# Optimization experiments

Hardware: AMD Instinct MI355X
Metric: run time of the kernel (lower is better)

Reference implementation:

```python
import jax, jax.numpy as jnp
import numpy as np

DIM = 1024
HEADS = 16
DIM_HEAD = 64
INNER = HEADS * DIM_HEAD  # 1024
MAX_LEN = 4096
BASE = 10000.0
EPS = 1.1920928955078125e-07  # torch.finfo(float32).eps (RMSNorm eps=None default)


def _rope_tables():
    t = np.arange(MAX_LEN, dtype=np.float32)
    inv_freq = 1.0 / (BASE ** (np.arange(0, DIM_HEAD, 2, dtype=np.float32) / DIM_HEAD))
    freqs = np.einsum('i,j->ij', t, inv_freq)          # [max_len, d/2]
    emb = np.concatenate([freqs, freqs], axis=-1)       # [max_len, d]
    return jnp.asarray(np.sin(emb)), jnp.asarray(np.cos(emb))


def setup_inputs() -> dict:
    key = jax.random.key(0)
    ks = jax.random.split(key, 5)
    x = jax.random.normal(ks[0], (2, 2048, DIM), dtype=jnp.float32)
    norm_w = jnp.ones((DIM,), dtype=jnp.float32)
    # store projection weights as [in, out] (transposed torch Linear weight)
    w_qkv = jax.random.normal(ks[1], (DIM, 3 * INNER), dtype=jnp.float32) * (DIM ** -0.5)
    w_o = jax.random.normal(ks[2], (INNER, DIM), dtype=jnp.float32) * (INNER ** -0.5)
    b_o = jax.random.normal(ks[3], (DIM,), dtype=jnp.float32) * 0.01
    sin, cos = _rope_tables()
    return {"x": x, "norm_w": norm_w, "w_qkv": w_qkv, "w_o": w_o, "b_o": b_o,
            "sin": sin, "cos": cos}


def _rotate_half(t):
    t1, t2 = jnp.split(t, 2, axis=-1)
    return jnp.concatenate([-t2, t1], axis=-1)


def _apply_rope(t, sin, cos):
    # t: [b, h, n, d]; sin/cos: [n, d]
    return t * cos + _rotate_half(t) * sin


def reference(x, norm_w, w_qkv, w_o, b_o, sin, cos):
    b, n, _ = x.shape
    # RMSNorm
    xn = x * jax.lax.rsqrt(jnp.mean(x * x, axis=-1, keepdims=True) + EPS) * norm_w
    # QKV projection
    qkv = xn @ w_qkv                                   # [b, n, 3*inner]
    q, k, v = jnp.split(qkv, 3, axis=-1)
    def to_heads(t):
        return t.reshape(b, n, HEADS, DIM_HEAD).transpose(0, 2, 1, 3)  # [b,h,n,d]
    q, k, v = to_heads(q), to_heads(k), to_heads(v)
    s, c = sin[:n], cos[:n]
    q = _apply_rope(q, s, c)
    k = _apply_rope(k, s, c)
    # causal SDPA
    scale = DIM_HEAD ** -0.5
    scores = jnp.einsum('bhqd,bhkd->bhqk', q, k) * scale
    causal = jnp.tril(jnp.ones((n, n), dtype=bool))
    scores = jnp.where(causal, scores, jnp.finfo(scores.dtype).min)
    attn = jax.nn.softmax(scores, axis=-1)
    out = jnp.einsum('bhqk,bhkd->bhqd', attn, v)
    out = out.transpose(0, 2, 1, 3).reshape(b, n, INNER)
    return out @ w_o + b_o
```

## Files before the change

### kernel.cpp

```cpp
#include <hip/hip_runtime.h>
#include <hip/hip_bf16.h>
#include <stdint.h>
#include <stddef.h>

#define NTOK   2048
#define NHEAD  16
#define DHEAD  64
#define DMODEL 1024
#define NROWS  4096
#define NQKV   3072
#define RMS_EPS 1.1920928955078125e-07f
#define QSCALE 0.1803368801111204f

typedef short bf16x8 __attribute__((ext_vector_type(8)));
typedef float f32x4  __attribute__((ext_vector_type(4)));
typedef unsigned short u16x4 __attribute__((ext_vector_type(4)));
typedef unsigned short u16x8 __attribute__((ext_vector_type(8)));

__device__ __forceinline__ unsigned short f2b(float f) {
  unsigned u = __builtin_bit_cast(unsigned, f);
  return (unsigned short)((u + 0x7fffu + ((u >> 16) & 1u)) >> 16);
}

__device__ __forceinline__ unsigned pk2bf(float a, float b) {
  __hip_bfloat162 h = __float22bfloat162_rn(make_float2(a, b));
  unsigned u;
  __builtin_memcpy(&u, &h, 4);
  return u;
}

__device__ __forceinline__ void gl16(const void* g, void* l) {
  __builtin_amdgcn_global_load_lds((__attribute__((address_space(1))) void*)g,
                                   (__attribute__((address_space(3))) void*)l,
                                   16, 0, 0);
}

__global__ __launch_bounds__(256) void k_rmsnorm(const float* __restrict__ x,
                                                 const float* __restrict__ w,
                                                 unsigned short* __restrict__ xn) {
  int row = blockIdx.x;
  int t = threadIdx.x;
  float4 v = ((const float4*)(x + (size_t)row * DMODEL))[t];
  float ss = v.x * v.x + v.y * v.y + v.z * v.z + v.w * v.w;
#pragma unroll
  for (int m = 1; m < 64; m <<= 1) ss += __shfl_xor(ss, m, 64);
  __shared__ float red[4];
  if ((t & 63) == 0) red[t >> 6] = ss;
  __syncthreads();
  float tot = (red[0] + red[1]) + (red[2] + red[3]);
  float rs = rsqrtf(tot * (1.0f / DMODEL) + RMS_EPS);
  float4 wv = ((const float4*)w)[t];
  u16x4 o;
  o.x = f2b(v.x * rs * wv.x);
  o.y = f2b(v.y * rs * wv.y);
  o.z = f2b(v.z * rs * wv.z);
  o.w = f2b(v.w * rs * wv.w);
  *(u16x4*)(xn + (size_t)row * DMODEL + t * 4) = o;
}

__global__ __launch_bounds__(256) void k_transpose_bf16(const float* __restrict__ W,
                                                        unsigned short* __restrict__ Wt,
                                                        int K, int Nw) {
  __shared__ float tile[64][65];
  int bk = blockIdx.x * 64;
  int bn = blockIdx.y * 64;
  int t = threadIdx.x;
  int tr = t >> 4;
  int tc = (t & 15) * 4;
#pragma unroll
  for (int rr = 0; rr < 64; rr += 16) {
    float4 v = *(const float4*)&W[(size_t)(bk + tr + rr) * Nw + bn + tc];
    tile[tr + rr][tc + 0] = v.x;
    tile[tr + rr][tc + 1] = v.y;
    tile[tr + rr][tc + 2] = v.z;
    tile[tr + rr][tc + 3] = v.w;
  }
  __syncthreads();
#pragma unroll
  for (int rr = 0; rr < 64; rr += 16) {
    int n = bn + tr + rr;
    u16x4 o;
    o.x = f2b(tile[tc + 0][tr + rr]);
    o.y = f2b(tile[tc + 1][tr + rr]);
    o.z = f2b(tile[tc + 2][tr + rr]);
    o.w = f2b(tile[tc + 3][tr + rr]);
    *(u16x4*)&Wt[(size_t)n * K + bk + tc] = o;
  }
}

__global__ __launch_bounds__(256) void k_qkv_gemm(
    const unsigned short* __restrict__ A, const unsigned short* __restrict__ Bt,
    const float* __restrict__ sin_t, const float* __restrict__ cos_t,
    unsigned short* __restrict__ Qh, unsigned short* __restrict__ Kh,
    unsigned short* __restrict__ Vh) {
  __shared__ unsigned short As[2][128 * 32];
  __shared__ unsigned short Bs[2][128 * 32];
  int bm = blockIdx.x, bn = blockIdx.y;
  int t = threadIdx.x;
  int l = t & 63, w = t >> 6;
  int wr = w >> 1, wc = w & 1;
  int lr = l & 15, lg = l >> 4;
  f32x4 acc[4][4] = {};

  int srow = t >> 2;
  int scho = (t & 3) * 8;
  const unsigned short* Ag = A + (size_t)(bm * 128 + srow) * DMODEL + scho;
  const unsigned short* Bg = Bt + (size_t)(bn * 128 + srow) * DMODEL + scho;

  gl16(Ag, &As[0][t * 8]);
  gl16(Ag + 64 * DMODEL, &As[0][(t + 256) * 8]);
  gl16(Bg, &Bs[0][t * 8]);
  gl16(Bg + 64 * DMODEL, &Bs[0][(t + 256) * 8]);
  __syncthreads();

  for (int i = 0; i < 32; i++) {
    int cur = i & 1, nxt = cur ^ 1;
    if (i < 31) {
      int k1 = (i + 1) * 32;
      gl16(Ag + k1, &As[nxt][t * 8]);
      gl16(Ag + k1 + 64 * DMODEL, &As[nxt][(t + 256) * 8]);
      gl16(Bg + k1, &Bs[nxt][t * 8]);
      gl16(Bg + k1 + 64 * DMODEL, &Bs[nxt][(t + 256) * 8]);
    }
    bf16x8 af[4], bfr[4];
#pragma unroll
    for (int ii = 0; ii < 4; ii++)
      af[ii] = *(const bf16x8*)&As[cur][(wr * 64 + ii * 16 + lr) * 32 + lg * 8];
#pragma unroll
    for (int jj = 0; jj < 4; jj++)
      bfr[jj] = *(const bf16x8*)&Bs[cur][(wc * 64 + jj * 16 + lr) * 32 + lg * 8];
#pragma unroll
    for (int ii = 0; ii < 4; ii++)
#pragma unroll
      for (int jj = 0; jj < 4; jj++)
        acc[ii][jj] = __builtin_amdgcn_mfma_f32_16x16x32_bf16(af[ii], bfr[jj], acc[ii][jj], 0, 0, 0);
    __syncthreads();
  }

  int nc0 = bn * 128 + wc * 64;
  int which = nc0 >> 10;
  int h = (nc0 & 1023) >> 6;
#pragma unroll
  for (int i = 0; i < 4; i++) {
#pragma unroll
    for (int r = 0; r < 4; r++) {
      int m = bm * 128 + wr * 64 + i * 16 + lg * 4 + r;
      int b = m >> 11;
      int n = m & (NTOK - 1);
      size_t obase = ((size_t)(b * NHEAD + h) * NTOK + n) * DHEAD;
      if (which == 2) {
#pragma unroll
        for (int j = 0; j < 4; j++) Vh[obase + j * 16 + lr] = f2b(acc[i][j][r]);
      } else {
        unsigned short* dst = which ? Kh : Qh;
        float qs = which ? 1.0f : QSCALE;
#pragma unroll
        for (int j = 0; j < 2; j++) {
          int d = j * 16 + lr;
          float t1 = acc[i][j][r];
          float t2 = acc[i][j + 2][r];
          float c1 = cos_t[n * DHEAD + d],      s1 = sin_t[n * DHEAD + d];
          float c2 = cos_t[n * DHEAD + d + 32], s2 = sin_t[n * DHEAD + d + 32];
          dst[obase + d]      = f2b((t1 * c1 - t2 * s1) * qs);
          dst[obase + d + 32] = f2b((t2 * c2 + t1 * s2) * qs);
        }
      }
    }
  }
}

#define SL(q, a, b) ((q) | ((a) << 6) | ((b) << 12))
__constant__ int SLOTS[48] = {
  SL(31,0,16), SL(31,16,32), SL(30,15,31), SL(15,0,16),
  SL(30,0,15), SL(29,0,15),  SL(29,15,30), SL(28,14,29), SL(14,0,15),
  SL(28,0,14), SL(27,0,14),  SL(27,14,28), SL(26,13,27), SL(13,0,14),
  SL(26,0,13), SL(25,0,13),  SL(25,13,26), SL(24,12,25), SL(12,0,13),
  SL(24,0,12), SL(23,0,12),  SL(23,12,24), SL(22,11,23), SL(11,0,12),
  SL(22,0,11), SL(21,0,11),  SL(21,11,22), SL(20,10,21), SL(10,0,11),
  SL(20,0,10), SL(19,0,10),  SL(19,10,20), SL(18,9,19),  SL(9,0,10),
  SL(18,0,9),  SL(17,0,9),   SL(17,9,18),  SL(16,8,17),  SL(8,0,9),
  SL(16,0,8),  SL(7,0,8),    SL(6,0,7),    SL(5,0,6),    SL(4,0,5),
  SL(3,0,4),   SL(2,0,3),    SL(1,0,2),    SL(0,0,1)
};

__global__ __launch_bounds__(256, 4) void k_attn(
    const unsigned short* __restrict__ Qh, const unsigned short* __restrict__ Kh,
    const unsigned short* __restrict__ Vh, unsigned short* __restrict__ AO,
    unsigned short* __restrict__ Opart, float* __restrict__ Mpart,
    float* __restrict__ Lpart) {
  int bh = blockIdx.x;
  int sv = SLOTS[blockIdx.y];
  int qt = sv & 63, kt0 = (sv >> 6) & 63, kt1 = sv >> 12;
  bool partial = (kt0 != 0) || (kt1 != qt + 1);
  int half = (kt0 != 0) ? 1 : 0;
  int t = threadIdx.x;
  int l = t & 63, w = t >> 6;
  int lr = l & 15, lg = l >> 4;

  __shared__ unsigned short Ks[2][64 * 64];
  __shared__ unsigned short Vt[2][64 * 64];
  __shared__ unsigned short Ps[4][16 * 64];

  const unsigned short* Qb = Qh + (size_t)bh * NTOK * DHEAD;
  const unsigned short* Kb = Kh + (size_t)bh * NTOK * DHEAD;
  const unsigned short* Vb = Vh + (size_t)bh * NTOK * DHEAD;

  int qrow = qt * 64 + w * 16 + lr;
  bf16x8 aq0 = *(const bf16x8*)&Qb[(size_t)qrow * DHEAD + lg * 8];
  bf16x8 aq1 = *(const bf16x8*)&Qb[(size_t)qrow * DHEAD + 32 + lg * 8];

  f32x4 accO[4] = {};
  float mrow = -1e38f;
  float lsum = 0.f;

  int srow = t >> 3;
  int spc  = t & 7;
  int vr0  = (t >> 3) * 2;

  {
    int kv0 = kt0 * 64;
    gl16(Kb + (size_t)(kv0 + srow) * DHEAD + (spc ^ (srow & 7)) * 8, &Ks[0][t * 8]);
    gl16(Kb + (size_t)(kv0 + srow + 32) * DHEAD + (spc ^ ((srow + 32) & 7)) * 8,
         &Ks[0][(t + 256) * 8]);
    bf16x8 v0 = *(const bf16x8*)&Vb[(size_t)(kv0 + vr0) * DHEAD + spc * 8];
    bf16x8 v1 = *(const bf16x8*)&Vb[(size_t)(kv0 + vr0 + 1) * DHEAD + spc * 8];
#pragma unroll
    for (int jj = 0; jj < 8; jj++) {
      int d = spc * 8 + jj;
      int sw = ((d & 7) ^ ((d >> 3) & 7)) << 4;
      unsigned pk = (unsigned)(unsigned short)v0[jj] | ((unsigned)(unsigned short)v1[jj] << 16);
      *(unsigned*)((char*)Vt[0] + d * 128 + ((vr0 * 2) ^ sw)) = pk;
    }
  }
  __syncthreads();

  for (int kt = kt0; kt < kt1; ++kt) {
    int cur = (kt - kt0) & 1, nxt = cur ^ 1;
    int kv0 = kt * 64;
    bool notlast = (kt + 1 < kt1);

    bf16x8 pv0, pv1;
    if (notlast) {
      int kvn = kv0 + 64;
      gl16(Kb + (size_t)(kvn + srow) * DHEAD + (spc ^ (srow & 7)) * 8, &Ks[nxt][t * 8]);
      gl16(Kb + (size_t)(kvn + srow + 32) * DHEAD + (spc ^ ((srow + 32) & 7)) * 8,
           &Ks[nxt][(t + 256) * 8]);
      pv0 = *(const bf16x8*)&Vb[(size_t)(kvn + vr0) * DHEAD + spc * 8];
      pv1 = *(const bf16x8*)&Vb[(size_t)(kvn + vr0 + 1) * DHEAD + spc * 8];
    }

    f32x4 s[4];
#pragma unroll
    for (int nf = 0; nf < 4; nf++) {
      int krow = nf * 16 + lr;
      const char* kbase = (const char*)Ks[cur] + krow * 128;
      bf16x8 bk0 = *(const bf16x8*)(kbase + ((lg * 16) ^ ((krow & 7) << 4)));
      bf16x8 bk1 = *(const bf16x8*)(kbase + ((lg * 16 + 64) ^ ((krow & 7) << 4)));
      f32x4 z = {};
      z = __builtin_amdgcn_mfma_f32_16x16x32_bf16(bk0, aq0, z, 0, 0, 0);
      s[nf] = __builtin_amdgcn_mfma_f32_16x16x32_bf16(bk1, aq1, z, 0, 0, 0);
    }

    if (kt == qt) {
      int qr = qt * 64 + w * 16 + lr;
#pragma unroll
      for (int nf = 0; nf < 4; nf++)
#pragma unroll
        for (int r = 0; r < 4; r++)
          if (kv0 + nf * 16 + lg * 4 + r > qr) s[nf][r] = -1e30f;
    }

    float t1m = fmaxf(fmaxf(s[0][0], s[0][1]), s[0][2]);
    float t2m = fmaxf(fmaxf(s[0][3], s[1][0]), s[1][1]);
    float t3m = fmaxf(fmaxf(s[1][2], s[1][3]), s[2][0]);
    float t4m = fmaxf(fmaxf(s[2][1], s[2][2]), s[2][3]);
    float t5m = fmaxf(fmaxf(s[3][0], s[3][1]), s[3][2]);
    float pm = fmaxf(fmaxf(fmaxf(t1m, t2m), t3m), fmaxf(fmaxf(t4m, t5m), s[3][3]));
    pm = fmaxf(pm, __shfl_xor(pm, 16, 64));
    pm = fmaxf(pm, __shfl_xor(pm, 32, 64));
    if (__any(pm > mrow + 8.0f)) {
      float mnew = fmaxf(mrow, pm);
      float corr = exp2f(mrow - mnew);
      mrow = mnew;
      lsum *= corr;
      float c0 = __shfl(corr, lg * 4 + 0, 64);
      float c1 = __shfl(corr, lg * 4 + 1, 64);
      float c2 = __shfl(corr, lg * 4 + 2, 64);
      float c3 = __shfl(corr, lg * 4 + 3, 64);
#pragma unroll
      for (int df = 0; df < 4; df++) {
        accO[df][0] *= c0; accO[df][1] *= c1;
        accO[df][2] *= c2; accO[df][3] *= c3;
      }
    }
    {
      float m = mrow;
      float sum = 0.f;
      char* pw = (char*)Ps[w] + lr * 128;
      int sw = (lr & 7) << 4;
#pragma unroll
      for (int nf = 0; nf < 4; nf++) {
        float p0 = exp2f(s[nf][0] - m);
        float p1 = exp2f(s[nf][1] - m);
        float p2 = exp2f(s[nf][2] - m);
        float p3 = exp2f(s[nf][3] - m);
        sum += (p0 + p1) + (p2 + p3);
        unsigned w0 = pk2bf(p0, p1);
        unsigned w1 = pk2bf(p2, p3);
        *(uint64_t*)(pw + ((nf * 32 + lg * 8) ^ sw)) = (uint64_t)w0 | ((uint64_t)w1 << 32);
      }
      sum += __shfl_xor(sum, 16, 64);
      sum += __shfl_xor(sum, 32, 64);
      lsum += sum;
    }

#pragma unroll
    for (int ks = 0; ks < 2; ks++) {
      const char* pb = (const char*)Ps[w] + lr * 128;
      bf16x8 ap = *(const bf16x8*)(pb + ((lg * 16 + ks * 64) ^ ((lr & 7) << 4)));
#pragma unroll
      for (int df = 0; df < 4; df++) {
        int col = df * 16 + lr;
        int sw = ((col & 7) ^ ((col >> 3) & 7)) << 4;
        bf16x8 bv = *(const bf16x8*)((const char*)Vt[cur] + col * 128 + ((lg * 16 + ks * 64) ^ sw));
        accO[df] = __builtin_amdgcn_mfma_f32_16x16x32_bf16(ap, bv, accO[df], 0, 0, 0);
      }
    }

    if (notlast) {
#pragma unroll
      for (int jj = 0; jj < 8; jj++) {
        int d = spc * 8 + jj;
        int sw = ((d & 7) ^ ((d >> 3) & 7)) << 4;
        unsigned pk = (unsigned)(unsigned short)pv0[jj] | ((unsigned)(unsigned short)pv1[jj] << 16);
        *(unsigned*)((char*)Vt[nxt] + d * 128 + ((vr0 * 2) ^ sw)) = pk;
      }
    }
    __syncthreads();
  }

  if (partial) {
    int pbase = (((bh << 4) + (qt - 16)) << 1) + half;
    if (lg == 0) {
      Mpart[pbase * 64 + w * 16 + lr] = mrow;
      Lpart[pbase * 64 + w * 16 + lr] = lsum;
    }
    unsigned short* Od = Opart + (size_t)pbase * 4096;
#pragma unroll
    for (int df = 0; df < 4; df++)
#pragma unroll
      for (int r = 0; r < 4; r++)
        Od[(w * 16 + lg * 4 + r) * 64 + df * 16 + lr] = f2b(accO[df][r]);
  } else {
    int b = bh >> 4, h = bh & 15;
    float li = 1.0f / lsum;
    float l0 = __shfl(li, lg * 4 + 0, 64);
    float l1 = __shfl(li, lg * 4 + 1, 64);
    float l2 = __shfl(li, lg * 4 + 2, 64);
    float l3 = __shfl(li, lg * 4 + 3, 64);
    int qbase = qt * 64 + w * 16;
#pragma unroll
    for (int df = 0; df < 4; df++) {
      int d = df * 16 + lr;
      size_t ob = ((size_t)(b * NTOK + qbase + lg * 4)) * DMODEL + h * DHEAD + d;
      AO[ob + 0 * DMODEL] = f2b(accO[df][0] * l0);
      AO[ob + 1 * DMODEL] = f2b(accO[df][1] * l1);
      AO[ob + 2 * DMODEL] = f2b(accO[df][2] * l2);
      AO[ob + 3 * DMODEL] = f2b(accO[df][3] * l3);
    }
  }
}

__global__ __launch_bounds__(256) void k_merge(const unsigned short* __restrict__ Opart,
                                               const float* __restrict__ Mpart,
                                               const float* __restrict__ Lpart,
                                               unsigned short* __restrict__ AO) {
  int bh = blockIdx.x, qq = blockIdx.y;
  int t = threadIdx.x;
  int row = t >> 2, d0 = (t & 3) << 4;
  int p0 = ((bh << 4) + qq) << 1;
  float m1 = Mpart[p0 * 64 + row],       l1 = Lpart[p0 * 64 + row];
  float m2 = Mpart[(p0 + 1) * 64 + row], l2 = Lpart[(p0 + 1) * 64 + row];
  float mm = fmaxf(m1, m2);
  float s1 = exp2f(m1 - mm), s2 = exp2f(m2 - mm);
  float li = 1.0f / (l1 * s1 + l2 * s2);
  float a1 = s1 * li, a2 = s2 * li;
  const unsigned short* O1 = Opart + (size_t)p0 * 4096 + row * 64 + d0;
  const unsigned short* O2 = O1 + 4096;
  int qt = 16 + qq;
  int b = bh >> 4, h = bh & 15;
  unsigned short* dst = AO + ((size_t)(b * NTOK + qt * 64 + row)) * DMODEL + h * DHEAD + d0;
#pragma unroll
  for (int c = 0; c < 2; c++) {
    u16x8 v1 = *(const u16x8*)(O1 + c * 8);
    u16x8 v2 = *(const u16x8*)(O2 + c * 8);
    u16x8 o;
#pragma unroll
    for (int e = 0; e < 8; e++) {
      float f1 = __builtin_bit_cast(float, (unsigned)v1[e] << 16);
      float g1 = __builtin_bit_cast(float, (unsigned)v2[e] << 16);
      o[e] = f2b(f1 * a1 + g1 * a2);
    }
    *(u16x8*)(dst + c * 8) = o;
  }
}

__global__ __launch_bounds__(256) void k_out_gemm(
    const unsigned short* __restrict__ A, const unsigned short* __restrict__ Bt,
    const float* __restrict__ bias, float* __restrict__ out) {
  __shared__ unsigned short As[2][128 * 32];
  __shared__ unsigned short Bs[2][64 * 32];
  int bm = blockIdx.x, bn = blockIdx.y;
  int t = threadIdx.x;
  int l = t & 63, w = t >> 6;
  int wr = w >> 1, wc = w & 1;
  int lr = l & 15, lg = l >> 4;
  f32x4 acc[4][2] = {};

  int srow = t >> 2;
  int scho = (t & 3) * 8;
  const unsigned short* Ag = A + (size_t)(bm * 128 + srow) * DMODEL + scho;
  const unsigned short* Bg = Bt + (size_t)(bn * 64 + srow) * DMODEL + scho;

  gl16(Ag, &As[0][t * 8]);
  gl16(Ag + 64 * DMODEL, &As[0][(t + 256) * 8]);
  if (srow < 64) gl16(Bg, &Bs[0][t * 8]);
  __syncthreads();

  for (int i = 0; i < 32; i++) {
    int cur = i & 1, nxt = cur ^ 1;
    if (i < 31) {
      int k1 = (i + 1) * 32;
      gl16(Ag + k1, &As[nxt][t * 8]);
      gl16(Ag + k1 + 64 * DMODEL, &As[nxt][(t + 256) * 8]);
      if (srow < 64) gl16(Bg + k1, &Bs[nxt][t * 8]);
    }
    bf16x8 af[4], bfr[2];
#pragma unroll
    for (int ii = 0; ii < 4; ii++)
      af[ii] = *(const bf16x8*)&As[cur][(wr * 64 + ii * 16 + lr) * 32 + lg * 8];
#pragma unroll
    for (int jj = 0; jj < 2; jj++)
      bfr[jj] = *(const bf16x8*)&Bs[cur][(wc * 32 + jj * 16 + lr) * 32 + lg * 8];
#pragma unroll
    for (int ii = 0; ii < 4; ii++)
#pragma unroll
      for (int jj = 0; jj < 2; jj++)
        acc[ii][jj] = __builtin_amdgcn_mfma_f32_16x16x32_bf16(af[ii], bfr[jj], acc[ii][jj], 0, 0, 0);
    __syncthreads();
  }
  int nc0 = bn * 64 + wc * 32;
#pragma unroll
  for (int i = 0; i < 4; i++)
#pragma unroll
    for (int r = 0; r < 4; r++) {
      int m = bm * 128 + wr * 64 + i * 16 + lg * 4 + r;
      float* orow = out + (size_t)m * DMODEL;
#pragma unroll
      for (int j = 0; j < 2; j++) {
        int col = nc0 + j * 16 + lr;
        orow[col] = acc[i][j][r] + bias[col];
      }
    }
}

extern "C" void kernel_launch(void* const* d_in, const int* in_sizes, int n_in,
                              void* d_out, int out_size, void* d_ws, size_t ws_size,
                              hipStream_t stream) {
  const float* x      = (const float*)d_in[0];
  const float* norm_w = (const float*)d_in[1];
  const float* w_qkv  = (const float*)d_in[2];
  const float* w_o    = (const float*)d_in[3];
  const float* b_o    = (const float*)d_in[4];
  const float* sin_t  = (const float*)d_in[5];
  const float* cos_t  = (const float*)d_in[6];
  float* out = (float*)d_out;

  char* ws = (char*)d_ws;
  unsigned short* xn    = (unsigned short*)(ws + (0u << 20));
  unsigned short* wqkvT = (unsigned short*)(ws + (8u << 20));
  unsigned short* woT   = (unsigned short*)(ws + (14u << 20));
  unsigned short* Qh    = (unsigned short*)(ws + (16u << 20));
  unsigned short* Kh    = (unsigned short*)(ws + (24u << 20));
  unsigned short* Vh    = (unsigned short*)(ws + (32u << 20));
  unsigned short* AO    = (unsigned short*)(ws + (40u << 20));
  unsigned short* Opart = (unsigned short*)(ws + (0u << 20));
  float*          Mpart = (float*)(ws + (8u << 20));
  float*          Lpart = (float*)(ws + (8u << 20) + (1u << 18));

  hipLaunchKernelGGL(k_rmsnorm, dim3(NROWS), dim3(256), 0, stream, x, norm_w, xn);
  hipLaunchKernelGGL(k_transpose_bf16, dim3(16, 48), dim3(256), 0, stream, w_qkv, wqkvT, DMODEL, NQKV);
  hipLaunchKernelGGL(k_transpose_bf16, dim3(16, 16), dim3(256), 0, stream, w_o, woT, DMODEL, DMODEL);
  hipLaunchKernelGGL(k_qkv_gemm, dim3(32, 24), dim3(256), 0, stream, xn, wqkvT, sin_t, cos_t, Qh, Kh, Vh);
  hipLaunchKernelGGL(k_attn, dim3(32, 48), dim3(256), 0, stream, Qh, Kh, Vh, AO, Opart, Mpart, Lpart);
  hipLaunchKernelGGL(k_merge, dim3(32, 16), dim3(256), 0, stream, Opart, Mpart, Lpart, AO);
  hipLaunchKernelGGL(k_out_gemm, dim3(32, 16), dim3(256), 0, stream, AO, woT, b_o, out);
}
```

Before: 120.0 us.

## Store V transposed from QKV GEMM and async-load it into attention LDS

The QKV GEMM epilogue now writes V in a [b,h,d,n] transposed layout, so the attention kernel can fetch V tiles with direct global-to-LDS loads using the same XOR swizzle as K. This replaces the register-staged V load and the per-element transpose scatter into LDS inside the loop. LDS offsets are precomputed outside the loop, and exp2f is replaced with the raw hardware exp2 instruction. The transposed V stores in the GEMM epilogue are strided by NTOK per element, which could make that epilogue slower.

After: 120.0 us. About the same (+0.0%).

```diff
diff --git a/kernel.cpp b/kernel.cpp
--- a/kernel.cpp
+++ b/kernel.cpp
@@ -27,6 +27,16 @@
   unsigned u;
   __builtin_memcpy(&u, &h, 4);
   return u;
+}
+
+__device__ __forceinline__ float fexp2(float x) {
+#if __has_builtin(__builtin_amdgcn_exp2f)
+  return __builtin_amdgcn_exp2f(x);
+#else
+  float r;
+  asm("v_exp_f32 %0, %1" : "=v"(r) : "v"(x));
+  return r;
+#endif
 }
 
 __device__ __forceinline__ void gl16(const void* g, void* l) {
@@ -92,7 +102,7 @@
     const unsigned short* __restrict__ A, const unsigned short* __restrict__ Bt,
     const float* __restrict__ sin_t, const float* __restrict__ cos_t,
     unsigned short* __restrict__ Qh, unsigned short* __restrict__ Kh,
-    unsigned short* __restrict__ Vh) {
+    unsigned short* __restrict__ VhT) {
   __shared__ unsigned short As[2][128 * 32];
   __shared__ unsigned short Bs[2][128 * 32];
   int bm = blockIdx.x, bn = blockIdx.y;
@@ -147,11 +157,14 @@
       int m = bm * 128 + wr * 64 + i * 16 + lg * 4 + r;
       int b = m >> 11;
       int n = m & (NTOK - 1);
-      size_t obase = ((size_t)(b * NHEAD + h) * NTOK + n) * DHEAD;
       if (which == 2) {
 #pragma unroll
-        for (int j = 0; j < 4; j++) Vh[obase + j * 16 + lr] = f2b(acc[i][j][r]);
+        for (int j = 0; j < 4; j++) {
+          int d = j * 16 + lr;
+          VhT[((size_t)((b * NHEAD + h) * DHEAD) + d) * NTOK + n] = f2b(acc[i][j][r]);
+        }
       } else {
+        size_t obase = ((size_t)(b * NHEAD + h) * NTOK + n) * DHEAD;
         unsigned short* dst = which ? Kh : Qh;
         float qs = which ? 1.0f : QSCALE;
 #pragma unroll
@@ -185,7 +198,7 @@
 
 __global__ __launch_bounds__(256, 4) void k_attn(
     const unsigned short* __restrict__ Qh, const unsigned short* __restrict__ Kh,
-    const unsigned short* __restrict__ Vh, unsigned short* __restrict__ AO,
+    const unsigned short* __restrict__ VhT, unsigned short* __restrict__ AO,
     unsigned short* __restrict__ Opart, float* __restrict__ Mpart,
     float* __restrict__ Lpart) {
   int bh = blockIdx.x;
@@ -198,12 +211,12 @@
   int lr = l & 15, lg = l >> 4;
 
   __shared__ unsigned short Ks[2][64 * 64];
-  __shared__ unsigned short Vt[2][64 * 64];
+  __shared__ unsigned short Vs[2][64 * 64];
   __shared__ unsigned short Ps[4][16 * 64];
 
-  const unsigned short* Qb = Qh + (size_t)bh * NTOK * DHEAD;
-  const unsigned short* Kb = Kh + (size_t)bh * NTOK * DHEAD;
-  const unsigned short* Vb = Vh + (size_t)bh * NTOK * DHEAD;
+  const unsigned short* Qb = Qh  + (size_t)bh * NTOK * DHEAD;
+  const unsigned short* Kb = Kh  + (size_t)bh * NTOK * DHEAD;
+  const unsigned short* Vb = VhT + (size_t)bh * DHEAD * NTOK;
 
   int qrow = qt * 64 + w * 16 + lr;
   bf16x8 aq0 = *(const bf16x8*)&Qb[(size_t)qrow * DHEAD + lg * 8];
@@ -215,47 +228,54 @@
 
   int srow = t >> 3;
   int spc  = t & 7;
-  int vr0  = (t >> 3) * 2;
+  int sc0  = (spc ^ (srow & 7)) * 8;
+  int sc1  = (spc ^ ((srow + 32) & 7)) * 8;
+
+  int koff[4][2], voff[2][4], poff[2], pwoff[4];
+#pragma unroll
+  for (int nf = 0; nf < 4; nf++) {
+    int krow = nf * 16 + lr;
+    koff[nf][0] = krow * 128 + ((lg * 16) ^ ((krow & 7) << 4));
+    koff[nf][1] = krow * 128 + ((lg * 16 + 64) ^ ((krow & 7) << 4));
+    pwoff[nf] = lr * 128 + ((nf * 32 + lg * 8) ^ ((lr & 7) << 4));
+  }
+#pragma unroll
+  for (int ks = 0; ks < 2; ks++) {
+    poff[ks] = lr * 128 + ((lg * 16 + ks * 64) ^ ((lr & 7) << 4));
+#pragma unroll
+    for (int df = 0; df < 4; df++) {
+      int col = df * 16 + lr;
+      voff[ks][df] = col * 128 + ((lg * 16 + ks * 64) ^ ((col & 7) << 4));
+    }
+  }
 
   {
     int kv0 = kt0 * 64;
-    gl16(Kb + (size_t)(kv0 + srow) * DHEAD + (spc ^ (srow & 7)) * 8, &Ks[0][t * 8]);
-    gl16(Kb + (size_t)(kv0 + srow + 32) * DHEAD + (spc ^ ((srow + 32) & 7)) * 8,
-         &Ks[0][(t + 256) * 8]);
-    bf16x8 v0 = *(const bf16x8*)&Vb[(size_t)(kv0 + vr0) * DHEAD + spc * 8];
-    bf16x8 v1 = *(const bf16x8*)&Vb[(size_t)(kv0 + vr0 + 1) * DHEAD + spc * 8];
-#pragma unroll
-    for (int jj = 0; jj < 8; jj++) {
-      int d = spc * 8 + jj;
-      int sw = ((d & 7) ^ ((d >> 3) & 7)) << 4;
-      unsigned pk = (unsigned)(unsigned short)v0[jj] | ((unsigned)(unsigned short)v1[jj] << 16);
-      *(unsigned*)((char*)Vt[0] + d * 128 + ((vr0 * 2) ^ sw)) = pk;
-    }
+    gl16(Kb + (size_t)(kv0 + srow) * DHEAD + sc0, &Ks[0][t * 8]);
+    gl16(Kb + (size_t)(kv0 + srow + 32) * DHEAD + sc1, &Ks[0][(t + 256) * 8]);
+    gl16(Vb + (size_t)srow * NTOK + kv0 + sc0, &Vs[0][t * 8]);
+    gl16(Vb + (size_t)(srow + 32) * NTOK + kv0 + sc1, &Vs[0][(t + 256) * 8]);
   }
   __syncthreads();
 
   for (int kt = kt0; kt < kt1; ++kt) {
     int cur = (kt - kt0) & 1, nxt = cur ^ 1;
     int kv0 = kt * 64;
-    bool notlast = (kt + 1 < kt1);
-
-    bf16x8 pv0, pv1;
-    if (notlast) {
+
+    if (kt + 1 < kt1) {
       int kvn = kv0 + 64;
-      gl16(Kb + (size_t)(kvn + srow) * DHEAD + (spc ^ (srow & 7)) * 8, &Ks[nxt][t * 8]);
-      gl16(Kb + (size_t)(kvn + srow + 32) * DHEAD + (spc ^ ((srow + 32) & 7)) * 8,
-           &Ks[nxt][(t + 256) * 8]);
-      pv0 = *(const bf16x8*)&Vb[(size_t)(kvn + vr0) * DHEAD + spc * 8];
-      pv1 = *(const bf16x8*)&Vb[(size_t)(kvn + vr0 + 1) * DHEAD + spc * 8];
-    }
-
+      gl16(Kb + (size_t)(kvn + srow) * DHEAD + sc0, &Ks[nxt][t * 8]);
+      gl16(Kb + (size_t)(kvn + srow + 32) * DHEAD + sc1, &Ks[nxt][(t + 256) * 8]);
+      gl16(Vb + (size_t)srow * NTOK + kvn + sc0, &Vs[nxt][t * 8]);
+      gl16(Vb + (size_t)(srow + 32) * NTOK + kvn + sc1, &Vs[nxt][(t + 256) * 8]);
+    }
+
+    const char* kb = (const char*)Ks[cur];
     f32x4 s[4];
 #pragma unroll
     for (int nf = 0; nf < 4; nf++) {
-      int krow = nf * 16 + lr;
-      const char* kbase = (const char*)Ks[cur] + krow * 128;
-      bf16x8 bk0 = *(const bf16x8*)(kbase + ((lg * 16) ^ ((krow & 7) << 4)));
-      bf16x8 bk1 = *(const bf16x8*)(kbase + ((lg * 16 + 64) ^ ((krow & 7) << 4)));
+      bf16x8 bk0 = *(const bf16x8*)(kb + koff[nf][0]);
+      bf16x8 bk1 = *(const bf16x8*)(kb + koff[nf][1]);
       f32x4 z = {};
       z = __builtin_amdgcn_mfma_f32_16x16x32_bf16(bk0, aq0, z, 0, 0, 0);
       s[nf] = __builtin_amdgcn_mfma_f32_16x16x32_bf16(bk1, aq1, z, 0, 0, 0);
@@ -280,7 +300,7 @@
     pm = fmaxf(pm, __shfl_xor(pm, 32, 64));
     if (__any(pm > mrow + 8.0f)) {
       float mnew = fmaxf(mrow, pm);
-      float corr = exp2f(mrow - mnew);
+      float corr = fexp2(mrow - mnew);
       mrow = mnew;
       lsum *= corr;
       float c0 = __shfl(corr, lg * 4 + 0, 64);
@@ -296,44 +316,32 @@
     {
       float m = mrow;
       float sum = 0.f;
-      char* pw = (char*)Ps[w] + lr * 128;
-      int sw = (lr & 7) << 4;
+      char* pw = (char*)Ps[w];
 #pragma unroll
       for (int nf = 0; nf < 4; nf++) {
-        float p0 = exp2f(s[nf][0] - m);
-        float p1 = exp2f(s[nf][1] - m);
-        float p2 = exp2f(s[nf][2] - m);
-        float p3 = exp2f(s[nf][3] - m);
+        float p0 = fexp2(s[nf][0] - m);
+        float p1 = fexp2(s[nf][1] - m);
+        float p2 = fexp2(s[nf][2] - m);
+        float p3 = fexp2(s[nf][3] - m);
         sum += (p0 + p1) + (p2 + p3);
         unsigned w0 = pk2bf(p0, p1);
         unsigned w1 = pk2bf(p2, p3);
-        *(uint64_t*)(pw + ((nf * 32 + lg * 8) ^ sw)) = (uint64_t)w0 | ((uint64_t)w1 << 32);
+        *(uint64_t*)(pw + pwoff[nf]) = (uint64_t)w0 | ((uint64_t)w1 << 32);
       }
       sum += __shfl_xor(sum, 16, 64);
       sum += __shfl_xor(sum, 32, 64);
       lsum += sum;
     }
 
+    const char* pb = (const char*)Ps[w];
+    const char* vb = (const char*)Vs[cur];
 #pragma unroll
     for (int ks = 0; ks < 2; ks++) {
-      const char* pb = (const char*)Ps[w] + lr * 128;
-      bf16x8 ap = *(const bf16x8*)(pb + ((lg * 16 + ks * 64) ^ ((lr & 7) << 4)));
+      bf16x8 ap = *(const bf16x8*)(pb + poff[ks]);
 #pragma unroll
       for (int df = 0; df < 4; df++) {
-        int col = df * 16 + lr;
-        int sw = ((col & 7) ^ ((col >> 3) & 7)) << 4;
-        bf16x8 bv = *(const bf16x8*)((const char*)Vt[cur] + col * 128 + ((lg * 16 + ks * 64) ^ sw));
+        bf16x8 bv = *(const bf16x8*)(vb + voff[ks][df]);
         accO[df] = __builtin_amdgcn_mfma_f32_16x16x32_bf16(ap, bv, accO[df], 0, 0, 0);
-      }
-    }
-
-    if (notlast) {
-#pragma unroll
-      for (int jj = 0; jj < 8; jj++) {
-        int d = spc * 8 + jj;
-        int sw = ((d & 7) ^ ((d >> 3) & 7)) << 4;
-        unsigned pk = (unsigned)(unsigned short)pv0[jj] | ((unsigned)(unsigned short)pv1[jj] << 16);
-        *(unsigned*)((char*)Vt[nxt] + d * 128 + ((vr0 * 2) ^ sw)) = pk;
       }
     }
     __syncthreads();
@@ -382,7 +390,7 @@
   float m1 = Mpart[p0 * 64 + row],       l1 = Lpart[p0 * 64 + row];
   float m2 = Mpart[(p0 + 1) * 64 + row], l2 = Lpart[(p0 + 1) * 64 + row];
   float mm = fmaxf(m1, m2);
-  float s1 = exp2f(m1 - mm), s2 = exp2f(m2 - mm);
+  float s1 = fexp2(m1 - mm), s2 = fexp2(m2 - mm);
   float li = 1.0f / (l1 * s1 + l2 * s2);
   float a1 = s1 * li, a2 = s2 * li;
   const unsigned short* O1 = Opart + (size_t)p0 * 4096 + row * 64 + d0;
@@ -482,7 +490,7 @@
   unsigned short* woT   = (unsigned short*)(ws + (14u << 20));
   unsigned short* Qh    = (unsigned short*)(ws + (16u << 20));
   unsigned short* Kh    = (unsigned short*)(ws + (24u << 20));
-  unsigned short* Vh    = (unsigned short*)(ws + (32u << 20));
+  unsigned short* VhT   = (unsigned short*)(ws + (32u << 20));
   unsigned short* AO    = (unsigned short*)(ws + (40u << 20));
   unsigned short* Opart = (unsigned short*)(ws + (0u << 20));
   float*          Mpart = (float*)(ws + (8u << 20));
@@ -491,8 +499,8 @@
   hipLaunchKernelGGL(k_rmsnorm, dim3(NROWS), dim3(256), 0, stream, x, norm_w, xn);
   hipLaunchKernelGGL(k_transpose_bf16, dim3(16, 48), dim3(256), 0, stream, w_qkv, wqkvT, DMODEL, NQKV);
   hipLaunchKernelGGL(k_transpose_bf16, dim3(16, 16), dim3(256), 0, stream, w_o, woT, DMODEL, DMODEL);
-  hipLaunchKernelGGL(k_qkv_gemm, dim3(32, 24), dim3(256), 0, stream, xn, wqkvT, sin_t, cos_t, Qh, Kh, Vh);
-  hipLaunchKernelGGL(k_attn, dim3(32, 48), dim3(256), 0, stream, Qh, Kh, Vh, AO, Opart, Mpart, Lpart);
+  hipLaunchKernelGGL(k_qkv_gemm, dim3(32, 24), dim3(256), 0, stream, xn, wqkvT, sin_t, cos_t, Qh, Kh, VhT);
+  hipLaunchKernelGGL(k_attn, dim3(32, 48), dim3(256), 0, stream, Qh, Kh, VhT, AO, Opart, Mpart, Lpart);
   hipLaunchKernelGGL(k_merge, dim3(32, 16), dim3(256), 0, stream, Opart, Mpart, Lpart, AO);
   hipLaunchKernelGGL(k_out_gemm, dim3(32, 16), dim3(256), 0, stream, AO, woT, b_o, out);
 }
```
